# Performance work log

Hardware: AMD Instinct MI355X
Metric: run time of the kernel (lower is better)

Reference implementation:

```python
import jax, jax.numpy as jnp
import numpy as np


def setup_inputs() -> dict:
    key = jax.random.key(0)
    k1, k2 = jax.random.split(key)
    B, T, V = 256, 128, 512
    x = jax.random.normal(k1, (B, T, V), dtype=jnp.float32)
    targets = jax.random.randint(k2, (B, T), 0, V)
    return {"x": x, "targets": targets, "sup_batchsize": 256}


def reference(x, targets, sup_batchsize):
    # Faithful vectorization of InfoNCELoss.loss_fun (the per-i Python loop).
    x = jnp.clip(x, -30.0, 30.0)
    B, T, V = x.shape
    S = int(sup_batchsize)
    tgt = targets[:S]  # [S, T] target sequences used as positives/negatives

    # terms[i, b] = sum_t x[b, t, tgt[i, t]]  (gather each target sequence across the whole batch)
    gathered = jnp.take_along_axis(x[None], tgt[:, None, :, None], axis=3)  # [S, B, T, 1]
    terms = gathered[..., 0].sum(axis=-1)  # [S, B]

    denom = jax.nn.logsumexp(terms, axis=1)  # [S]
    numerators = terms[jnp.arange(S), jnp.arange(S)]  # terms[i, i] = own-sequence score
    losses = numerators - denom  # [S], per-row InfoNCE log-prob

    # coef[i, b] = 1{b == i} - softmax_b(terms[i, :])
    indicator = (jnp.arange(B)[None, :] == jnp.arange(S)[:, None]).astype(x.dtype)
    coef = indicator - jax.nn.softmax(terms, axis=1)  # [S, B]

    # grad[b, t, v] = sum_i 1{v == tgt[i, t]} * coef[i, b]  (scatter-add, no [S,T,V] one-hot)
    t_idx = jnp.arange(T)[None, :]  # broadcasts with tgt to [S, T]
    grad = jnp.zeros_like(x).at[:, t_idx, tgt].add(
        jnp.broadcast_to(coef.T[:, :, None], (B, S, T))
    )

    total_loss = losses.sum()  # InfoNCEFunction.forward returns sum(loss)
    return total_loss, grad
```

## Files before the change

### kernel.cpp

```cpp
#include <hip/hip_runtime.h>


#define BB 256
#define TT 128
#define VV 512
#define SS 256
#define QSPLIT 4
#define TQ (TT / QSPLIT)
#define TC 8

__global__ __launch_bounds__(256) void terms_kernel(
    const float* __restrict__ x, const int* __restrict__ tgt,
    float* __restrict__ partial) {
  int bid = blockIdx.x;
  int b = bid & 255;
  int q = bid >> 8;
  int s = threadIdx.x;
  __shared__ float xch[TC * VV];
  float acc = 0.f;
  const float* xb = x + ((size_t)b * TT + (size_t)q * TQ) * VV;
#pragma unroll 1
  for (int c = 0; c < TQ / TC; ++c) {
    const float4* src = (const float4*)(xb + c * TC * VV);
    float4* dst = (float4*)xch;
#pragma unroll
    for (int k = 0; k < 4; ++k) {
      float4 v = src[s + k * 256];
      v.x = fminf(fmaxf(v.x, -30.f), 30.f);
      v.y = fminf(fmaxf(v.y, -30.f), 30.f);
      v.z = fminf(fmaxf(v.z, -30.f), 30.f);
      v.w = fminf(fmaxf(v.w, -30.f), 30.f);
      dst[s + k * 256] = v;
    }
    int t0 = q * TQ + c * TC;
    const int4 tg0 = *(const int4*)(tgt + s * TT + t0);
    const int4 tg1 = *(const int4*)(tgt + s * TT + t0 + 4);
    __syncthreads();
    acc += xch[0 * VV + tg0.x];
    acc += xch[1 * VV + tg0.y];
    acc += xch[2 * VV + tg0.z];
    acc += xch[3 * VV + tg0.w];
    acc += xch[4 * VV + tg1.x];
    acc += xch[5 * VV + tg1.y];
    acc += xch[6 * VV + tg1.z];
    acc += xch[7 * VV + tg1.w];
    __syncthreads();
  }
  partial[(((size_t)q << 8) + b) * 256 + s] = acc;
}

__global__ __launch_bounds__(256) void softmax_kernel(
    const float* __restrict__ partial, float* __restrict__ coefT,
    float* __restrict__ losses) {
  int s = blockIdx.x;
  int b = threadIdx.x;
  float t = 0.f;
#pragma unroll
  for (int q = 0; q < QSPLIT; ++q)
    t += partial[(((size_t)q << 8) + b) * 256 + s];
  __shared__ float red[256];
  red[b] = t;
  __syncthreads();
#pragma unroll
  for (int off = 128; off > 0; off >>= 1) {
    if (b < off) red[b] = fmaxf(red[b], red[b + off]);
    __syncthreads();
  }
  float m = red[0];
  __syncthreads();
  float e = expf(t - m);
  red[b] = e;
  __syncthreads();
#pragma unroll
  for (int off = 128; off > 0; off >>= 1) {
    if (b < off) red[b] += red[b + off];
    __syncthreads();
  }
  float sum = red[0];
  coefT[(b << 8) + s] = (b == s ? 1.f : 0.f) - e / sum;
  if (b == s) losses[s] = t - (m + logf(sum));
}

__global__ __launch_bounds__(256) void grad_kernel(
    const float* __restrict__ coefT, const int* __restrict__ tgt,
    const float* __restrict__ losses, float* __restrict__ out) {
  int bid = blockIdx.x;
  int b = bid & 255;
  int q = bid >> 8;
  int s = threadIdx.x;
  __shared__ float rows[TC * VV];
  if (bid == 0) {
    __shared__ double red[256];
    red[s] = (double)losses[s];
    __syncthreads();
    for (int off = 128; off > 0; off >>= 1) {
      if (s < off) red[s] += red[s + off];
      __syncthreads();
    }
    if (s == 0) out[0] = (float)red[0];
  }
  float c = coefT[(b << 8) + s];
  float* gb = out + 1 + ((size_t)b * TT + (size_t)q * TQ) * VV;
#pragma unroll 1
  for (int ch = 0; ch < TQ / TC; ++ch) {
    float4* rz = (float4*)rows;
#pragma unroll
    for (int k = 0; k < 4; ++k)
      rz[s + k * 256] = make_float4(0.f, 0.f, 0.f, 0.f);
    int t0 = q * TQ + ch * TC;
    const int4 tg0 = *(const int4*)(tgt + s * TT + t0);
    const int4 tg1 = *(const int4*)(tgt + s * TT + t0 + 4);
    __syncthreads();
    atomicAdd(&rows[0 * VV + tg0.x], c);
    atomicAdd(&rows[1 * VV + tg0.y], c);
    atomicAdd(&rows[2 * VV + tg0.z], c);
    atomicAdd(&rows[3 * VV + tg0.w], c);
    atomicAdd(&rows[4 * VV + tg1.x], c);
    atomicAdd(&rows[5 * VV + tg1.y], c);
    atomicAdd(&rows[6 * VV + tg1.z], c);
    atomicAdd(&rows[7 * VV + tg1.w], c);
    __syncthreads();
    float* dsto = gb + ch * TC * VV;
#pragma unroll
    for (int k = 0; k < 16; ++k)
      dsto[s + k * 256] = rows[s + k * 256];
    __syncthreads();
  }
}

extern "C" void kernel_launch(void* const* d_in, const int* in_sizes, int n_in,
                              void* d_out, int out_size, void* d_ws, size_t ws_size,
                              hipStream_t stream) {
  const float* x = (const float*)d_in[0];
  const int* tgt = (const int*)d_in[1];
  float* out = (float*)d_out;

  float* partial = (float*)d_ws;
  float* coefT = partial + QSPLIT * 256 * 256;
  float* losses = coefT + 256 * 256;

  terms_kernel<<<dim3(256 * QSPLIT), dim3(256), 0, stream>>>(x, tgt, partial);
  softmax_kernel<<<dim3(256), dim3(256), 0, stream>>>(partial, coefT, losses);
  grad_kernel<<<dim3(256 * QSPLIT), dim3(256), 0, stream>>>(coefT, tgt, losses, out);
}
```

Before: 175.8 us.

## Align grad output stores with shifted shared tile and split terms kernel wider

The grad kernel now has one block per 8-row chunk and writes into a shared tile shifted by one float. The output at out+1 is misaligned, and the shift lets the tile go out as aligned float4 nontemporal stores. The boundary element is picked up from the previous chunk's last column, and the total loss is folded into block 0's first slot. The terms kernel splits T into 8 parts and preloads its targets, and the softmax uses wavefront shuffle reductions. This removes unaligned scalar stores and serial chunk loops, at the cost of extra boundary-handling logic.

```diff
diff --git a/kernel.cpp b/kernel.cpp
--- a/kernel.cpp
+++ b/kernel.cpp
@@ -1,26 +1,28 @@
 #include <hip/hip_runtime.h>
 
 
-#define BB 256
 #define TT 128
 #define VV 512
-#define SS 256
-#define QSPLIT 4
+#define QSPLIT 8
 #define TQ (TT / QSPLIT)
 #define TC 8
+
+typedef float f4 __attribute__((ext_vector_type(4)));
 
 __global__ __launch_bounds__(256) void terms_kernel(
     const float* __restrict__ x, const int* __restrict__ tgt,
     float* __restrict__ partial) {
   int bid = blockIdx.x;
-  int b = bid & 255;
-  int q = bid >> 8;
-  int s = threadIdx.x;
-  __shared__ float xch[TC * VV];
+  int b = bid & 255, q = bid >> 8, s = threadIdx.x;
+  __shared__ __align__(16) float xch[TC * VV];
+  const float* xb = x + ((size_t)b * TT + q * TQ) * VV;
+  int4 tg[4];
+#pragma unroll
+  for (int k = 0; k < 4; ++k)
+    tg[k] = ((const int4*)(tgt + (size_t)s * TT + q * TQ))[k];
   float acc = 0.f;
-  const float* xb = x + ((size_t)b * TT + (size_t)q * TQ) * VV;
-#pragma unroll 1
-  for (int c = 0; c < TQ / TC; ++c) {
+#pragma unroll
+  for (int c = 0; c < 2; ++c) {
     const float4* src = (const float4*)(xb + c * TC * VV);
     float4* dst = (float4*)xch;
 #pragma unroll
@@ -32,100 +34,97 @@
       v.w = fminf(fmaxf(v.w, -30.f), 30.f);
       dst[s + k * 256] = v;
     }
-    int t0 = q * TQ + c * TC;
-    const int4 tg0 = *(const int4*)(tgt + s * TT + t0);
-    const int4 tg1 = *(const int4*)(tgt + s * TT + t0 + 4);
     __syncthreads();
-    acc += xch[0 * VV + tg0.x];
-    acc += xch[1 * VV + tg0.y];
-    acc += xch[2 * VV + tg0.z];
-    acc += xch[3 * VV + tg0.w];
-    acc += xch[4 * VV + tg1.x];
-    acc += xch[5 * VV + tg1.y];
-    acc += xch[6 * VV + tg1.z];
-    acc += xch[7 * VV + tg1.w];
+    int4 a0 = tg[2 * c], a1 = tg[2 * c + 1];
+    acc += xch[0 * VV + a0.x] + xch[1 * VV + a0.y] +
+           xch[2 * VV + a0.z] + xch[3 * VV + a0.w] +
+           xch[4 * VV + a1.x] + xch[5 * VV + a1.y] +
+           xch[6 * VV + a1.z] + xch[7 * VV + a1.w];
     __syncthreads();
   }
-  partial[(((size_t)q << 8) + b) * 256 + s] = acc;
+  partial[(size_t)((q << 8) + b) * 256 + s] = acc;
 }
 
 __global__ __launch_bounds__(256) void softmax_kernel(
     const float* __restrict__ partial, float* __restrict__ coefT,
     float* __restrict__ losses) {
-  int s = blockIdx.x;
-  int b = threadIdx.x;
+  int s = blockIdx.x, b = threadIdx.x;
+  int w = b >> 6, lane = b & 63;
   float t = 0.f;
 #pragma unroll
   for (int q = 0; q < QSPLIT; ++q)
-    t += partial[(((size_t)q << 8) + b) * 256 + s];
-  __shared__ float red[256];
-  red[b] = t;
+    t += partial[(size_t)((q << 8) + b) * 256 + s];
+  float m = t;
+#pragma unroll
+  for (int off = 32; off; off >>= 1) m = fmaxf(m, __shfl_xor(m, off));
+  __shared__ float wm[4], ws[4];
+  if (lane == 0) wm[w] = m;
   __syncthreads();
+  m = fmaxf(fmaxf(wm[0], wm[1]), fmaxf(wm[2], wm[3]));
+  float e = expf(t - m);
+  float ss = e;
 #pragma unroll
-  for (int off = 128; off > 0; off >>= 1) {
-    if (b < off) red[b] = fmaxf(red[b], red[b + off]);
-    __syncthreads();
-  }
-  float m = red[0];
+  for (int off = 32; off; off >>= 1) ss += __shfl_xor(ss, off);
+  if (lane == 0) ws[w] = ss;
   __syncthreads();
-  float e = expf(t - m);
-  red[b] = e;
-  __syncthreads();
-#pragma unroll
-  for (int off = 128; off > 0; off >>= 1) {
-    if (b < off) red[b] += red[b + off];
-    __syncthreads();
-  }
-  float sum = red[0];
+  float sum = ws[0] + ws[1] + ws[2] + ws[3];
   coefT[(b << 8) + s] = (b == s ? 1.f : 0.f) - e / sum;
-  if (b == s) losses[s] = t - (m + logf(sum));
+  if (b == s) losses[s] = (t - m) - logf(sum);
 }
 
 __global__ __launch_bounds__(256) void grad_kernel(
     const float* __restrict__ coefT, const int* __restrict__ tgt,
     const float* __restrict__ losses, float* __restrict__ out) {
-  int bid = blockIdx.x;
-  int b = bid & 255;
-  int q = bid >> 8;
-  int s = threadIdx.x;
-  __shared__ float rows[TC * VV];
-  if (bid == 0) {
-    __shared__ double red[256];
-    red[s] = (double)losses[s];
-    __syncthreads();
-    for (int off = 128; off > 0; off >>= 1) {
-      if (s < off) red[s] += red[s + off];
-      __syncthreads();
-    }
-    if (s == 0) out[0] = (float)red[0];
+  int j = blockIdx.x, s = threadIdx.x;
+  int w = s >> 6, lane = s & 63;
+  int b = j >> 4, t0 = (j & 15) << 3;
+  __shared__ __align__(16) float rows[TC * VV + 1];
+  __shared__ double dred[4];
+  f4* rz = (f4*)rows;
+  f4 zero = {0.f, 0.f, 0.f, 0.f};
+#pragma unroll
+  for (int k = 0; k < 4; ++k) rz[s + k * 256] = zero;
+  if (s == 0) rows[TC * VV] = 0.f;
+
+  float c = coefT[(b << 8) + s];
+  int4 tg0 = *(const int4*)(tgt + (size_t)s * TT + t0);
+  int4 tg1 = *(const int4*)(tgt + (size_t)s * TT + t0 + 4);
+
+  float bc = 0.f;
+  if (j > 0) {
+    int R = j * 8 - 1;
+    int bh = R >> 7, th = R & 127;
+    if (tgt[(size_t)s * TT + th] == VV - 1) bc = coefT[(bh << 8) + s];
   }
-  float c = coefT[(b << 8) + s];
-  float* gb = out + 1 + ((size_t)b * TT + (size_t)q * TQ) * VV;
-#pragma unroll 1
-  for (int ch = 0; ch < TQ / TC; ++ch) {
-    float4* rz = (float4*)rows;
+  double ls = 0.0;
+  if (j == 0) ls = (double)losses[s];
+
+  __syncthreads();
+  atomicAdd(&rows[1 + 0 * VV + tg0.x], c);
+  atomicAdd(&rows[1 + 1 * VV + tg0.y], c);
+  atomicAdd(&rows[1 + 2 * VV + tg0.z], c);
+  atomicAdd(&rows[1 + 3 * VV + tg0.w], c);
+  atomicAdd(&rows[1 + 4 * VV + tg1.x], c);
+  atomicAdd(&rows[1 + 5 * VV + tg1.y], c);
+  atomicAdd(&rows[1 + 6 * VV + tg1.z], c);
+  atomicAdd(&rows[1 + 7 * VV + tg1.w], c);
 #pragma unroll
-    for (int k = 0; k < 4; ++k)
-      rz[s + k * 256] = make_float4(0.f, 0.f, 0.f, 0.f);
-    int t0 = q * TQ + ch * TC;
-    const int4 tg0 = *(const int4*)(tgt + s * TT + t0);
-    const int4 tg1 = *(const int4*)(tgt + s * TT + t0 + 4);
-    __syncthreads();
-    atomicAdd(&rows[0 * VV + tg0.x], c);
-    atomicAdd(&rows[1 * VV + tg0.y], c);
-    atomicAdd(&rows[2 * VV + tg0.z], c);
-    atomicAdd(&rows[3 * VV + tg0.w], c);
-    atomicAdd(&rows[4 * VV + tg1.x], c);
-    atomicAdd(&rows[5 * VV + tg1.y], c);
-    atomicAdd(&rows[6 * VV + tg1.z], c);
-    atomicAdd(&rows[7 * VV + tg1.w], c);
-    __syncthreads();
-    float* dsto = gb + ch * TC * VV;
+  for (int off = 32; off; off >>= 1) bc += __shfl_xor(bc, off);
+  if (j > 0 && lane == 0) atomicAdd(&rows[0], bc);
+  if (j == 0) {
 #pragma unroll
-    for (int k = 0; k < 16; ++k)
-      dsto[s + k * 256] = rows[s + k * 256];
-    __syncthreads();
+    for (int off = 32; off; off >>= 1) ls += __shfl_xor(ls, off);
+    if (lane == 0) dred[w] = ls;
   }
+  __syncthreads();
+  if (j == 0 && s == 0) rows[0] = (float)(dred[0] + dred[1] + dred[2] + dred[3]);
+  __syncthreads();
+
+  f4* go = (f4*)(out + (size_t)j * 4096);
+#pragma unroll
+  for (int k = 0; k < 4; ++k)
+    __builtin_nontemporal_store(rz[s + k * 256], &go[s + k * 256]);
+  if (j == 4095 && s == 0) out[(size_t)4096 * 4096] = rows[TC * VV];
 }
 
 extern "C" void kernel_launch(void* const* d_in, const int* in_sizes, int n_in,
@@ -139,7 +138,7 @@
   float* coefT = partial + QSPLIT * 256 * 256;
   float* losses = coefT + 256 * 256;
 
-  terms_kernel<<<dim3(256 * QSPLIT), dim3(256), 0, stream>>>(x, tgt, partial);
+  terms_kernel<<<dim3(2048), dim3(256), 0, stream>>>(x, tgt, partial);
   softmax_kernel<<<dim3(256), dim3(256), 0, stream>>>(partial, coefT, losses);
-  grad_kernel<<<dim3(256 * QSPLIT), dim3(256), 0, stream>>>(coefT, tgt, losses, out);
+  grad_kernel<<<dim3(4096), dim3(256), 0, stream>>>(coefT, tgt, losses, out);
 }
```

After: 165.4 us. 1.06x faster.
